# Performance work log

Hardware: AMD Instinct MI355X
Metric: run time of the kernel (lower is better)

Reference implementation:

```python
import jax, jax.numpy as jnp
import numpy as np

C = 256
NUM_HEADS = 4
REDUCTION = 4
RED = C // REDUCTION           # 64
HEAD_DIM = RED // NUM_HEADS    # 16
SCALE = HEAD_DIM ** -0.5
LN_EPS = 1e-5


def setup_inputs() -> dict:
    key = jax.random.key(0)
    ks = jax.random.split(key, 9)
    B, H, W = 2, 64, 64
    x = jax.random.normal(ks[0], (B, C, H, W), dtype=jnp.float32)
    # LayerNorm params
    norm_w = jnp.ones((C,), jnp.float32)
    norm_b = jnp.zeros((C,), jnp.float32)
    # Linear weights (torch layout: [out, in]), y = x @ W.T
    qkv_w = jax.random.normal(ks[1], (3 * RED, C), jnp.float32) * (C ** -0.5)
    out_w = jax.random.normal(ks[2], (C, RED), jnp.float32) * (RED ** -0.5)
    # 1x1 conv weights, stored as [out_c, in_c]
    conv1_w = jax.random.normal(ks[3], (C // 2, C), jnp.float32) * (C ** -0.5)
    conv1_b = jax.random.normal(ks[4], (C // 2,), jnp.float32) * 0.01
    conv2_w = jax.random.normal(ks[5], (1, C // 2), jnp.float32) * ((C // 2) ** -0.5)
    conv2_b = jax.random.normal(ks[6], (1,), jnp.float32) * 0.01
    gamma = jnp.ones((1,), jnp.float32) * 0.5  # nonzero so output depends on attention
    return {"x": x, "norm_w": norm_w, "norm_b": norm_b, "qkv_w": qkv_w,
            "out_w": out_w, "conv1_w": conv1_w, "conv1_b": conv1_b,
            "conv2_w": conv2_w, "conv2_b": conv2_b, "gamma": gamma}


def reference(x, norm_w, norm_b, qkv_w, out_w, conv1_w, conv1_b, conv2_w, conv2_b, gamma):
    B, C_, H, W = x.shape
    N = H * W
    # [B, N, C]
    xf = x.reshape(B, C_, N).transpose(0, 2, 1)
    # LayerNorm over channel dim
    mu = jnp.mean(xf, axis=-1, keepdims=True)
    var = jnp.mean(jnp.square(xf - mu), axis=-1, keepdims=True)
    xn = (xf - mu) * jax.lax.rsqrt(var + LN_EPS) * norm_w + norm_b
    # QKV projection -> [B, N, 3*RED]
    qkv = jnp.einsum('bnc,oc->bno', xn, qkv_w)
    q, k, v = jnp.split(qkv, 3, axis=-1)
    def heads(t):  # [B, N, RED] -> [B, h, N, d]
        return t.reshape(B, N, NUM_HEADS, HEAD_DIM).transpose(0, 2, 1, 3)
    q, k, v = heads(q), heads(k), heads(v)
    attn = jax.nn.softmax(jnp.einsum('bhnd,bhmd->bhnm', q, k) * SCALE, axis=-1)
    # dynamic weight branch: two 1x1 convs on raw x
    d1 = jax.nn.relu(jnp.einsum('oc,bchw->bohw', conv1_w, x) + conv1_b[None, :, None, None])
    dyn = (jnp.einsum('oc,bchw->bohw', conv2_w, d1) + conv2_b[None, :, None, None])  # [B,1,H,W]
    dyn = dyn.reshape(B, 1, N)  # broadcast over heads
    # per-query row scaling of attention
    attn = attn * dyn[:, :, :, None]
    out = jnp.einsum('bhnm,bhmd->bhnd', attn, v)            # [B,h,N,d]
    out = out.transpose(0, 2, 1, 3).reshape(B, N, RED)      # [B,N,RED]
    out = jnp.einsum('bnr,cr->bnc', out, out_w)             # [B,N,C]
    out = out.transpose(0, 2, 1).reshape(B, C_, H, W)
    return jax.nn.sigmoid(gamma[0] * out + x)
```

## Files before the change

### kernel.cpp

```cpp
#include <hip/hip_runtime.h>
#include <cstdint>
#include <cstddef>

#define LOG2E 1.44269504088896340736f

typedef float  f32x16 __attribute__((ext_vector_type(16)));
typedef __bf16 bf16x8 __attribute__((ext_vector_type(8)));

union BF8 { bf16x8 v; uint u[4]; ushort us[8]; };

__device__ __forceinline__ uint pack_bf(float a, float b) {
    uint ua = __float_as_uint(a) + 0x8000u;
    uint ub = __float_as_uint(b) + 0x8000u;
    return __builtin_amdgcn_perm(ub, ua, 0x07060302u);
}
__device__ __forceinline__ float bf_lo(uint u) { return __uint_as_float(u << 16); }
__device__ __forceinline__ float bf_hi(uint u) { return __uint_as_float(u & 0xFFFF0000u); }

__global__ __launch_bounds__(256) void convert_w_kernel(
    const float* __restrict__ qkv_w, const float* __restrict__ c1w,
    const float* __restrict__ out_w,
    ushort* __restrict__ qkvw_b, ushort* __restrict__ c1w_b, ushort* __restrict__ ow_b)
{
    const int g = (blockIdx.x * 256 + threadIdx.x) * 4;
    const float* src; ushort* dst; int off; float sc = 1.f;
    if (g < 49152)      { src = qkv_w; dst = qkvw_b; off = g;
                          if (g < 16384) sc = 0.25f * LOG2E; }
    else if (g < 81920) { src = c1w;   dst = c1w_b;  off = g - 49152; }
    else                { src = out_w; dst = ow_b;   off = g - 81920; }
    float4 v = *(const float4*)(src + off);
    uint2 pk;
    pk.x = pack_bf(v.x * sc, v.y * sc);
    pk.y = pack_bf(v.z * sc, v.w * sc);
    *(uint2*)(dst + off) = pk;
}

__global__ __launch_bounds__(1024) void lnqkv_kernel(
    const float* __restrict__ x, const float* __restrict__ nw, const float* __restrict__ nb,
    const ushort* __restrict__ qkvw_b, const ushort* __restrict__ c1w_b,
    const float* __restrict__ c1b, const float* __restrict__ c2w,
    const float* __restrict__ c2b,
    ushort* __restrict__ Qb, ushort* __restrict__ Kb, ushort* __restrict__ Vsw,
    float* __restrict__ dynb)
{
    __shared__ union {
        struct {
            uint  XN[32 * 32 * 4];
            uint  XR[32 * 32 * 4];
            float red1[1024];
            float red2[1024];
        } p;
        float trans[10][33 * 32];
    } S;
    __shared__ float muS[32], rsS[32];
    __shared__ float dpart[4][32];

    const int t    = threadIdx.x;
    const int pg   = blockIdx.x;
    const int b    = pg >> 7;
    const int n0   = (pg & 127) * 32;

    {
        const int j  = t & 31;
        const int cg = t >> 5;
        const size_t xb = (size_t)b * 256 * 4096 + n0 + j;
        float v[8];
        #pragma unroll
        for (int i = 0; i < 8; ++i) v[i] = x[xb + (size_t)(cg * 8 + i) * 4096];
        float s1 = 0.f, s2 = 0.f;
        #pragma unroll
        for (int i = 0; i < 8; ++i) { s1 += v[i]; s2 += v[i] * v[i]; }
        uint4 pk;
        pk.x = pack_bf(v[0], v[1]); pk.y = pack_bf(v[2], v[3]);
        pk.z = pack_bf(v[4], v[5]); pk.w = pack_bf(v[6], v[7]);
        *(uint4*)&S.p.XR[(cg * 32 + j) * 4] = pk;
        S.p.red1[t] = s1; S.p.red2[t] = s2;
        __syncthreads();
        if (t < 32) {
            float a = 0.f, q = 0.f;
            #pragma unroll 8
            for (int g2 = 0; g2 < 32; ++g2) { a += S.p.red1[g2 * 32 + t]; q += S.p.red2[g2 * 32 + t]; }
            float mu  = a * (1.f / 256.f);
            float var = q * (1.f / 256.f) - mu * mu;
            muS[t] = mu; rsS[t] = rsqrtf(fmaxf(var, 0.f) + 1e-5f);
        }
        __syncthreads();
        const float mu = muS[j], rs = rsS[j];
        const float4 w0 = *(const float4*)(nw + cg * 8);
        const float4 w1 = *(const float4*)(nw + cg * 8 + 4);
        const float4 b0 = *(const float4*)(nb + cg * 8);
        const float4 b1 = *(const float4*)(nb + cg * 8 + 4);
        float e0 = (v[0] - mu) * rs * w0.x + b0.x;
        float e1 = (v[1] - mu) * rs * w0.y + b0.y;
        float e2 = (v[2] - mu) * rs * w0.z + b0.z;
        float e3 = (v[3] - mu) * rs * w0.w + b0.w;
        float e4 = (v[4] - mu) * rs * w1.x + b1.x;
        float e5 = (v[5] - mu) * rs * w1.y + b1.y;
        float e6 = (v[6] - mu) * rs * w1.z + b1.z;
        float e7 = (v[7] - mu) * rs * w1.w + b1.w;
        uint4 o;
        o.x = pack_bf(e0, e1); o.y = pack_bf(e2, e3);
        o.z = pack_bf(e4, e5); o.w = pack_bf(e6, e7);
        *(uint4*)&S.p.XN[(cg * 32 + j) * 4] = o;
    }
    __syncthreads();

    const int w    = t >> 6;
    const int lane = t & 63;
    const int m    = lane & 31;
    const int h    = lane >> 5;
    const ushort* xnB = (const ushort*)S.p.XN;
    const ushort* xrB = (const ushort*)S.p.XR;

    f32x16 acc;
    #pragma unroll
    for (int i = 0; i < 16; ++i) acc[i] = 0.f;

    if (w < 6) {
        const int qkv = w >> 1;
        const int ti  = w & 1;
        const ushort* ap = qkvw_b + (size_t)(qkv * 64 + ti * 32 + m) * 256 + h * 8;
        #pragma unroll 4
        for (int ks = 0; ks < 16; ++ks) {
            bf16x8 bf = *(const bf16x8*)(xnB + ((ks * 2 + h) * 32 + m) * 8);
            bf16x8 af = *(const bf16x8*)(ap + ks * 16);
            acc = __builtin_amdgcn_mfma_f32_32x32x16_bf16(af, bf, acc, 0, 0, 0);
        }
    } else if (w < 10) {
        const int ti = w - 6;
        const ushort* ap = c1w_b + (size_t)(ti * 32 + m) * 256 + h * 8;
        #pragma unroll 4
        for (int ks = 0; ks < 16; ++ks) {
            bf16x8 bf = *(const bf16x8*)(xrB + ((ks * 2 + h) * 32 + m) * 8);
            bf16x8 af = *(const bf16x8*)(ap + ks * 16);
            acc = __builtin_amdgcn_mfma_f32_32x32x16_bf16(af, bf, acc, 0, 0, 0);
        }
    }
    __syncthreads();

    if (w < 10) {
        float* tr = S.trans[w];
        #pragma unroll
        for (int r = 0; r < 16; ++r)
            tr[((r & 3) + 8 * (r >> 2) + 4 * h) * 33 + m] = acc[r];

        if (w < 4) {
            const int qkv = w >> 1, ti = w & 1;
            ushort* dst = (qkv == 0) ? Qb : Kb;
            #pragma unroll
            for (int it = 0; it < 2; ++it) {
                int unit = it * 2 + h;
                int hl = unit >> 1, half = unit & 1;
                float v0 = tr[(hl * 16 + half * 8 + 0) * 33 + m];
                float v1 = tr[(hl * 16 + half * 8 + 1) * 33 + m];
                float v2 = tr[(hl * 16 + half * 8 + 2) * 33 + m];
                float v3 = tr[(hl * 16 + half * 8 + 3) * 33 + m];
                float v4 = tr[(hl * 16 + half * 8 + 4) * 33 + m];
                float v5 = tr[(hl * 16 + half * 8 + 5) * 33 + m];
                float v6 = tr[(hl * 16 + half * 8 + 6) * 33 + m];
                float v7 = tr[(hl * 16 + half * 8 + 7) * 33 + m];
                uint4 pk;
                pk.x = pack_bf(v0, v1); pk.y = pack_bf(v2, v3);
                pk.z = pack_bf(v4, v5); pk.w = pack_bf(v6, v7);
                int head = ti * 2 + hl;
                *(uint4*)(dst + ((size_t)(b * 4 + head) * 4096 + n0 + m) * 16 + half * 8) = pk;
            }
        } else if (w < 6) {
            const int ti = w & 1;
            int d = lane & 15, u = lane >> 4;
            #pragma unroll
            for (int it = 0; it < 4; ++it) {
                int unit = it * 4 + u;
                int hl = unit >> 3, sg = unit & 7;
                float v0 = tr[(hl * 16 + d) * 33 + sg * 4 + 0];
                float v1 = tr[(hl * 16 + d) * 33 + sg * 4 + 1];
                float v2 = tr[(hl * 16 + d) * 33 + sg * 4 + 2];
                float v3 = tr[(hl * 16 + d) * 33 + sg * 4 + 3];
                uint2 pk; pk.x = pack_bf(v0, v1); pk.y = pack_bf(v2, v3);
                int head = ti * 2 + hl;
                *(uint2*)(Vsw + (((size_t)(b * 4 + head) * 1024 + (pg & 127) * 8 + sg) * 16 + d) * 4) = pk;
            }
        } else {
            const int ti = w - 6;
            float partial = 0.f;
            #pragma unroll
            for (int i = 0; i < 16; ++i) {
                int og = ti * 32 + h * 16 + i;
                partial += fmaxf(tr[(h * 16 + i) * 33 + m] + c1b[og], 0.f) * c2w[og];
            }
            float tot = partial + __shfl_xor(partial, 32);
            if (lane < 32) dpart[ti][m] = tot;
        }
    }
    __syncthreads();
    if (t < 32)
        dynb[(size_t)b * 4096 + n0 + t] =
            c2b[0] + dpart[0][t] + dpart[1][t] + dpart[2][t] + dpart[3][t];
}

__global__ __launch_bounds__(1024) void attn_final_kernel(
    const ushort* __restrict__ Qb, const ushort* __restrict__ Kb,
    const ushort* __restrict__ Vsw, const float* __restrict__ dynb,
    const ushort* __restrict__ ow_b, const float* __restrict__ x,
    const float* __restrict__ gamma, float* __restrict__ out)
{
    __shared__ float2 OM[4][4][8][32];
    __shared__ float  LM[4][4][32];

    const int t    = threadIdx.x;
    const int w    = t >> 6;
    const int lane = t & 63;
    const int c    = lane & 31;
    const int h    = lane >> 5;
    const int hd   = w & 3;
    const int kb   = w >> 2;
    const int pg   = blockIdx.x;
    const int b    = pg >> 7;
    const int n0   = (pg & 127) * 32;
    const int bh   = b * 4 + hd;

    const bf16x8 qf = *(const bf16x8*)(Qb + ((size_t)bh * 4096 + n0 + c) * 16 + h * 8);

    f32x16 oacc, zf;
    #pragma unroll
    for (int i = 0; i < 16; ++i) { oacc[i] = 0.f; zf[i] = 0.f; }

    const ushort* kp = Kb + ((size_t)bh * 4096 + kb * 1024 + c) * 16 + h * 8;
    const ushort* vb = Vsw + (size_t)bh * 65536 + ((size_t)kb * 256 + h) * 64 + c * 4;

    #pragma unroll 2
    for (int ch = 0; ch < 32; ++ch) {
        const bf16x8 kf = *(const bf16x8*)kp;
        f32x16 s = __builtin_amdgcn_mfma_f32_32x32x16_bf16(kf, qf, zf, 0, 0, 0);

        BF8 p1, p2;
        #pragma unroll
        for (int jj = 0; jj < 4; ++jj) {
            p1.u[jj] = pack_bf(__builtin_amdgcn_exp2f(s[2*jj]),   __builtin_amdgcn_exp2f(s[2*jj+1]));
            p2.u[jj] = pack_bf(__builtin_amdgcn_exp2f(s[8+2*jj]), __builtin_amdgcn_exp2f(s[8+2*jj+1]));
        }

        BF8 a1, a2;
        if (c < 16) {
            const uint2 g1 = *(const uint2*)(vb);
            const uint2 g2 = *(const uint2*)(vb + 128);
            const uint2 g3 = *(const uint2*)(vb + 256);
            const uint2 g4 = *(const uint2*)(vb + 384);
            a1.u[0] = g1.x; a1.u[1] = g1.y; a1.u[2] = g2.x; a1.u[3] = g2.y;
            a2.u[0] = g3.x; a2.u[1] = g3.y; a2.u[2] = g4.x; a2.u[3] = g4.y;
        } else {
            const uint f = (c == 16) ? 0x3F803F80u : 0u;
            a1.u[0] = a1.u[1] = a1.u[2] = a1.u[3] = f;
            a2.u[0] = a2.u[1] = a2.u[2] = a2.u[3] = f;
        }

        oacc = __builtin_amdgcn_mfma_f32_32x32x16_bf16(a1.v, p1.v, oacc, 0, 0, 0);
        oacc = __builtin_amdgcn_mfma_f32_32x32x16_bf16(a2.v, p2.v, oacc, 0, 0, 0);

        kp += 512; vb += 512;
    }

    OM[kb][hd][2 * h + 0][c] = make_float2(oacc[0], oacc[1]);
    OM[kb][hd][2 * h + 1][c] = make_float2(oacc[2], oacc[3]);
    OM[kb][hd][4 + 2 * h][c] = make_float2(oacc[4], oacc[5]);
    OM[kb][hd][5 + 2 * h][c] = make_float2(oacc[6], oacc[7]);
    if (h == 0) LM[kb][hd][c] = oacc[8];
    __syncthreads();

    if (w < 8) {
        const int m = c;
        const float dyn_px = dynb[(size_t)b * 4096 + n0 + m];

        f32x16 acc;
        #pragma unroll
        for (int i = 0; i < 16; ++i) acc[i] = 0.f;

        #pragma unroll
        for (int ks = 0; ks < 4; ++ks) {
            float l = LM[0][ks][m] + LM[1][ks][m] + LM[2][ks][m] + LM[3][ks][m];
            float fac = dyn_px / l;
            BF8 bfr;
            #pragma unroll
            for (int i = 0; i < 4; ++i) {
                int sl = 4 * h + i;
                float2 s0 = OM[0][ks][sl][m];
                float2 s1 = OM[1][ks][sl][m];
                float2 s2 = OM[2][ks][sl][m];
                float2 s3 = OM[3][ks][sl][m];
                float e0 = (s0.x + s1.x + s2.x + s3.x) * fac;
                float e1 = (s0.y + s1.y + s2.y + s3.y) * fac;
                bfr.u[i] = pack_bf(e0, e1);
            }
            bf16x8 af = *(const bf16x8*)(ow_b + (size_t)(w * 32 + m) * 64 + ks * 16 + h * 8);
            acc = __builtin_amdgcn_mfma_f32_32x32x16_bf16(af, bfr.v, acc, 0, 0, 0);
        }

        const float g = gamma[0];
        #pragma unroll
        for (int r = 0; r < 16; ++r) {
            int o = (r & 3) + 8 * (r >> 2) + 4 * h;
            size_t idx = ((size_t)b * 256 + w * 32 + o) * 4096 + n0 + m;
            float z = g * acc[r] + x[idx];
            out[idx] = 1.f / (1.f + __builtin_amdgcn_exp2f(-z * LOG2E));
        }
    }
}

extern "C" void kernel_launch(void* const* d_in, const int* in_sizes, int n_in,
                              void* d_out, int out_size, void* d_ws, size_t ws_size,
                              hipStream_t stream)
{
    const float* x      = (const float*)d_in[0];
    const float* norm_w = (const float*)d_in[1];
    const float* norm_b = (const float*)d_in[2];
    const float* qkv_w  = (const float*)d_in[3];
    const float* out_w  = (const float*)d_in[4];
    const float* c1w    = (const float*)d_in[5];
    const float* c1b    = (const float*)d_in[6];
    const float* c2w    = (const float*)d_in[7];
    const float* c2b    = (const float*)d_in[8];
    const float* gamma  = (const float*)d_in[9];

    char* ws = (char*)d_ws;
    ushort* Qb     = (ushort*)ws;
    ushort* Kb     = Qb + 524288;
    ushort* Vsw    = Kb + 524288;
    ushort* qkvw_b = Vsw + 524288;
    ushort* c1w_b  = qkvw_b + 49152;
    ushort* ow_b   = c1w_b + 32768;
    float*  dynb   = (float*)(ws + 3342336);

    hipLaunchKernelGGL(convert_w_kernel, dim3(96), dim3(256), 0, stream,
                       qkv_w, c1w, out_w, qkvw_b, c1w_b, ow_b);
    hipLaunchKernelGGL(lnqkv_kernel, dim3(256), dim3(1024), 0, stream,
                       x, norm_w, norm_b, qkvw_b, c1w_b, c1b, c2w, c2b,
                       Qb, Kb, Vsw, dynb);
    hipLaunchKernelGGL(attn_final_kernel, dim3(256), dim3(1024), 0, stream,
                       Qb, Kb, Vsw, dynb, ow_b, x, gamma, (float*)d_out);
}
```

Measured before the change: 114.8 us.

## Software-pipeline K/V register prefetch in attention loop, use hardware bf16 pack

Restructures the main attention loop so K fragments are loaded four iterations ahead and V fragments two iterations ahead, rotating through register buffers. The goal is to hide global-load latency behind the MFMA and exp work. The manual round-to-nearest bf16 packing is replaced with the v_cvt_pk_bf16_f32 instruction, and s_setprio raises wave priority around the MFMAs. The launch bounds now request 4 blocks per CU, which may cap registers enough to cause spills. The prefetch also reads past the end of each head's K/V range on the final iterations, and those values go unused.

```diff
diff --git a/kernel.cpp b/kernel.cpp
--- a/kernel.cpp
+++ b/kernel.cpp
@@ -13,6 +13,11 @@
     uint ua = __float_as_uint(a) + 0x8000u;
     uint ub = __float_as_uint(b) + 0x8000u;
     return __builtin_amdgcn_perm(ub, ua, 0x07060302u);
+}
+__device__ __forceinline__ uint cvt_pk_bf(float a, float b) {
+    uint r;
+    asm("v_cvt_pk_bf16_f32 %0, %1, %2" : "=v"(r) : "v"(a), "v"(b));
+    return r;
 }
 __device__ __forceinline__ float bf_lo(uint u) { return __uint_as_float(u << 16); }
 __device__ __forceinline__ float bf_hi(uint u) { return __uint_as_float(u & 0xFFFF0000u); }
@@ -198,7 +203,7 @@
             c2b[0] + dpart[0][t] + dpart[1][t] + dpart[2][t] + dpart[3][t];
 }
 
-__global__ __launch_bounds__(1024) void attn_final_kernel(
+__global__ __launch_bounds__(1024, 4) void attn_final_kernel(
     const ushort* __restrict__ Qb, const ushort* __restrict__ Kb,
     const ushort* __restrict__ Vsw, const float* __restrict__ dynb,
     const ushort* __restrict__ ow_b, const float* __restrict__ x,
@@ -228,37 +233,59 @@
     const ushort* kp = Kb + ((size_t)bh * 4096 + kb * 1024 + c) * 16 + h * 8;
     const ushort* vb = Vsw + (size_t)bh * 65536 + ((size_t)kb * 256 + h) * 64 + c * 4;
 
-    #pragma unroll 2
-    for (int ch = 0; ch < 32; ++ch) {
-        const bf16x8 kf = *(const bf16x8*)kp;
-        f32x16 s = __builtin_amdgcn_mfma_f32_32x32x16_bf16(kf, qf, zf, 0, 0, 0);
-
-        BF8 p1, p2;
-        #pragma unroll
-        for (int jj = 0; jj < 4; ++jj) {
-            p1.u[jj] = pack_bf(__builtin_amdgcn_exp2f(s[2*jj]),   __builtin_amdgcn_exp2f(s[2*jj+1]));
-            p2.u[jj] = pack_bf(__builtin_amdgcn_exp2f(s[8+2*jj]), __builtin_amdgcn_exp2f(s[8+2*jj+1]));
-        }
-
-        BF8 a1, a2;
-        if (c < 16) {
-            const uint2 g1 = *(const uint2*)(vb);
-            const uint2 g2 = *(const uint2*)(vb + 128);
-            const uint2 g3 = *(const uint2*)(vb + 256);
-            const uint2 g4 = *(const uint2*)(vb + 384);
-            a1.u[0] = g1.x; a1.u[1] = g1.y; a1.u[2] = g2.x; a1.u[3] = g2.y;
-            a2.u[0] = g3.x; a2.u[1] = g3.y; a2.u[2] = g4.x; a2.u[3] = g4.y;
-        } else {
-            const uint f = (c == 16) ? 0x3F803F80u : 0u;
-            a1.u[0] = a1.u[1] = a1.u[2] = a1.u[3] = f;
-            a2.u[0] = a2.u[1] = a2.u[2] = a2.u[3] = f;
-        }
-
-        oacc = __builtin_amdgcn_mfma_f32_32x32x16_bf16(a1.v, p1.v, oacc, 0, 0, 0);
-        oacc = __builtin_amdgcn_mfma_f32_32x32x16_bf16(a2.v, p2.v, oacc, 0, 0, 0);
-
-        kp += 512; vb += 512;
-    }
+    BF8 cones;
+    {
+        const uint f = (c == 16) ? 0x3F803F80u : 0u;
+        cones.u[0] = f; cones.u[1] = f; cones.u[2] = f; cones.u[3] = f;
+    }
+
+    bf16x8 k0 = *(const bf16x8*)kp; kp += 512;
+    bf16x8 k1 = *(const bf16x8*)kp; kp += 512;
+    bf16x8 k2 = *(const bf16x8*)kp; kp += 512;
+    bf16x8 k3 = *(const bf16x8*)kp; kp += 512;
+    uint2 vA0 = *(const uint2*)(vb),       vB0 = *(const uint2*)(vb + 128);
+    uint2 vC0 = *(const uint2*)(vb + 256), vD0 = *(const uint2*)(vb + 384);
+    vb += 512;
+    uint2 vA1 = *(const uint2*)(vb),       vB1 = *(const uint2*)(vb + 128);
+    uint2 vC1 = *(const uint2*)(vb + 256), vD1 = *(const uint2*)(vb + 384);
+    vb += 512;
+
+#define STEP(K, VA, VB, VC, VD)                                                      \
+    {                                                                                \
+        __builtin_amdgcn_s_setprio(1);                                               \
+        f32x16 s = __builtin_amdgcn_mfma_f32_32x32x16_bf16(K, qf, zf, 0, 0, 0);      \
+        __builtin_amdgcn_s_setprio(0);                                               \
+        K = *(const bf16x8*)kp; kp += 512;                                           \
+        BF8 p1, p2;                                                                  \
+        p1.u[0] = cvt_pk_bf(__builtin_amdgcn_exp2f(s[0]),  __builtin_amdgcn_exp2f(s[1]));  \
+        p1.u[1] = cvt_pk_bf(__builtin_amdgcn_exp2f(s[2]),  __builtin_amdgcn_exp2f(s[3]));  \
+        p1.u[2] = cvt_pk_bf(__builtin_amdgcn_exp2f(s[4]),  __builtin_amdgcn_exp2f(s[5]));  \
+        p1.u[3] = cvt_pk_bf(__builtin_amdgcn_exp2f(s[6]),  __builtin_amdgcn_exp2f(s[7]));  \
+        p2.u[0] = cvt_pk_bf(__builtin_amdgcn_exp2f(s[8]),  __builtin_amdgcn_exp2f(s[9]));  \
+        p2.u[1] = cvt_pk_bf(__builtin_amdgcn_exp2f(s[10]), __builtin_amdgcn_exp2f(s[11])); \
+        p2.u[2] = cvt_pk_bf(__builtin_amdgcn_exp2f(s[12]), __builtin_amdgcn_exp2f(s[13])); \
+        p2.u[3] = cvt_pk_bf(__builtin_amdgcn_exp2f(s[14]), __builtin_amdgcn_exp2f(s[15])); \
+        BF8 a1, a2;                                                                  \
+        if (c < 16) {                                                                \
+            a1.u[0] = VA.x; a1.u[1] = VA.y; a1.u[2] = VB.x; a1.u[3] = VB.y;          \
+            a2.u[0] = VC.x; a2.u[1] = VC.y; a2.u[2] = VD.x; a2.u[3] = VD.y;          \
+        } else { a1 = cones; a2 = cones; }                                           \
+        VA = *(const uint2*)(vb);       VB = *(const uint2*)(vb + 128);              \
+        VC = *(const uint2*)(vb + 256); VD = *(const uint2*)(vb + 384);              \
+        vb += 512;                                                                   \
+        __builtin_amdgcn_s_setprio(1);                                               \
+        oacc = __builtin_amdgcn_mfma_f32_32x32x16_bf16(a1.v, p1.v, oacc, 0, 0, 0);   \
+        oacc = __builtin_amdgcn_mfma_f32_32x32x16_bf16(a2.v, p2.v, oacc, 0, 0, 0);   \
+        __builtin_amdgcn_s_setprio(0);                                               \
+    }
+
+    for (int it = 0; it < 8; ++it) {
+        STEP(k0, vA0, vB0, vC0, vD0);
+        STEP(k1, vA1, vB1, vC1, vD1);
+        STEP(k2, vA0, vB0, vC0, vD0);
+        STEP(k3, vA1, vB1, vC1, vD1);
+    }
+#undef STEP
 
     OM[kb][hd][2 * h + 0][c] = make_float2(oacc[0], oacc[1]);
     OM[kb][hd][2 * h + 1][c] = make_float2(oacc[2], oacc[3]);
```

Result: no change. 113.5 us (-1.2%).
